# Performance work log

Measured on AMD Instinct MI355X. Metric: run time of the kernel, lower is better.

Reference implementation:

```python
import jax, jax.numpy as jnp
import numpy as np

N_EMBD = 1024
N_HEAD = 16
HEAD_DIM = N_EMBD // N_HEAD


def setup_inputs() -> dict:
    key = jax.random.key(0)
    k1, k2, k3, k4, k5 = jax.random.split(key, 5)
    x = jax.random.normal(k1, (4, 2048, N_EMBD), dtype=jnp.float32)
    s = 1.0 / np.sqrt(N_EMBD)
    W_attn = jax.random.normal(k2, (N_EMBD, 3 * N_EMBD), dtype=jnp.float32) * s
    b_attn = jnp.zeros((3 * N_EMBD,), dtype=jnp.float32)
    W_proj = jax.random.normal(k3, (N_EMBD, N_EMBD), dtype=jnp.float32) * s
    b_proj = jnp.zeros((N_EMBD,), dtype=jnp.float32)
    return {"x": x, "W_attn": W_attn, "b_attn": b_attn, "W_proj": W_proj, "b_proj": b_proj}


def _attention(x, W_attn, b_attn, W_proj, b_proj):
    B, T, C = x.shape
    qkv = jnp.einsum("btc,cd->btd", x, W_attn) + b_attn  # [B,T,3C]
    q, k, v = jnp.split(qkv, 3, axis=-1)
    # [B,T,C] -> [B,H,T,D]
    def heads(t):
        return t.reshape(B, T, N_HEAD, HEAD_DIM).transpose(0, 2, 1, 3)
    q, k, v = heads(q), heads(k), heads(v)
    scale = 1.0 / np.sqrt(HEAD_DIM)
    scores = jnp.einsum("bhqd,bhkd->bhqk", q, k) * scale  # [B,H,T,T]
    causal = jnp.tril(jnp.ones((T, T), dtype=bool))
    scores = jnp.where(causal, scores, jnp.finfo(scores.dtype).min)
    attn = jax.nn.softmax(scores, axis=-1)
    y = jnp.einsum("bhqk,bhkd->bhqd", attn, v)  # [B,H,T,D]
    y = y.transpose(0, 2, 1, 3).reshape(B, T, C)
    return jnp.einsum("btc,cd->btd", y, W_proj) + b_proj


def reference(x, W_attn, b_attn, W_proj, b_proj):
    return _attention(x, W_attn, b_attn, W_proj, b_proj)
```

## Files before the change

kernel.cpp:

```cpp
#include <hip/hip_runtime.h>
#include <hip/hip_bf16.h>

#define BB 4
#define TT 2048
#define CC 1024
#define HH 16
#define DD 64
#define BT (BB*TT)
#define C3 (3*CC)
#define LDST 72
#define QSCALE 0.18033688011112042f

typedef __attribute__((ext_vector_type(8))) short short8;
typedef __attribute__((ext_vector_type(4))) float f32x4;

__device__ __forceinline__ short f2bs(float f) {
  __hip_bfloat16 h = __float2bfloat16(f);
  return *reinterpret_cast<short*>(&h);
}

__device__ __forceinline__ void gl_lds16(const short* g, short* l) {
  __builtin_amdgcn_global_load_lds(
      (const __attribute__((address_space(1))) void*)(g),
      (__attribute__((address_space(3))) void*)(l), 16, 0, 0);
}

__global__ __launch_bounds__(256)
void prep(const float* __restrict__ Wa, short* __restrict__ Wat,
          const float* __restrict__ Wp, short* __restrict__ Wpt,
          const float* __restrict__ x, short* __restrict__ Xb)
{
  __shared__ float Lt[64][65];
  const int bx = blockIdx.x;
  if (bx >= 64) {
    size_t chunk = (size_t)(bx - 64) * 16 + blockIdx.y;
    size_t i = (chunk * 256 + threadIdx.x) * 8;
    float4 a = *reinterpret_cast<const float4*>(x + i);
    float4 b = *reinterpret_cast<const float4*>(x + i + 4);
    short8 o;
    o[0] = f2bs(a.x); o[1] = f2bs(a.y); o[2] = f2bs(a.z); o[3] = f2bs(a.w);
    o[4] = f2bs(b.x); o[5] = f2bs(b.y); o[6] = f2bs(b.z); o[7] = f2bs(b.w);
    *reinterpret_cast<short8*>(Xb + i) = o;
    return;
  }
  const bool isA = (bx < 48);
  const float* in  = isA ? Wa  : Wp;
  short*       out = isA ? Wat : Wpt;
  const int N  = isA ? C3 : CC;
  const int n0 = (isA ? bx : bx - 48) * 64;
  const int k0 = blockIdx.y * 64;
  const int cx = threadIdx.x & 15, rr = threadIdx.x >> 4;
#pragma unroll
  for (int p = 0; p < 4; ++p) {
    int kr = p * 16 + rr;
    float4 u = *reinterpret_cast<const float4*>(in + (size_t)(k0 + kr) * N + n0 + cx * 4);
    Lt[kr][cx * 4 + 0] = u.x;
    Lt[kr][cx * 4 + 1] = u.y;
    Lt[kr][cx * 4 + 2] = u.z;
    Lt[kr][cx * 4 + 3] = u.w;
  }
  __syncthreads();
#pragma unroll
  for (int p = 0; p < 4; ++p) {
    int nr = p * 16 + rr;
    short4 o;
    o.x = f2bs(Lt[cx * 4 + 0][nr]);
    o.y = f2bs(Lt[cx * 4 + 1][nr]);
    o.z = f2bs(Lt[cx * 4 + 2][nr]);
    o.w = f2bs(Lt[cx * 4 + 3][nr]);
    *reinterpret_cast<short4*>(out + (size_t)(n0 + nr) * CC + k0 + cx * 4) = o;
  }
}

template<bool QKV, int NBF>
__global__ __launch_bounds__(512, 2)
void gemm256(const short* __restrict__ A, const short* __restrict__ Bt,
             const float* __restrict__ bias,
             short* __restrict__ qb, short* __restrict__ kb, short* __restrict__ vb,
             float* __restrict__ out)
{
  constexpr int BQ   = NBF * 64 * 32;
  constexpr int BOFF = 32768;
  __shared__ __align__(16) short SMEM[BOFF + 4 * BQ];

  const int t = threadIdx.x;
  const int lane = t & 63;
  const int l16 = lane & 15, quad = lane >> 4;
  const int w = t >> 6;
  const int wr = w >> 2, wc = w & 3;

  const int per   = gridDim.x >> 3;
  const int chunk = (blockIdx.x & 7) * per + (blockIdx.x >> 3);
  const int NBC   = QKV ? 12 : (CC / (NBF * 64));
  const int brow  = chunk / NBC, bcol = chunk % NBC;
  const int row0  = brow * 256;
  const int col0  = bcol * (NBF * 64);

  auto stageQA = [&](int bufS, int kcS, int tileS) __attribute__((always_inline)) {
#pragma unroll
    for (int l = 0; l < 2; ++l) {
      int gq = l * 512 + t;
      int rq = gq >> 2;
      int g  = (gq & 3) ^ ((rq >> 1) & 3);
      gl_lds16(A + (size_t)(row0 + rq) * CC + tileS * 64 + kcS * 32 + g * 8,
               &SMEM[bufS * 16384 + kcS * 8192 + gq * 8]);
    }
  };
  auto stageQB = [&](int bufS, int kcS, int tileS) __attribute__((always_inline)) {
#pragma unroll
    for (int l = 0; l < NBF / 2; ++l) {
      int gq = l * 512 + t;
      int rq = gq >> 2;
      int g  = (gq & 3) ^ ((rq >> 1) & 3);
      gl_lds16(Bt + (size_t)(col0 + rq) * CC + tileS * 64 + kcS * 32 + g * 8,
               &SMEM[BOFF + bufS * 2 * BQ + kcS * BQ + gq * 8]);
    }
  };

  f32x4 acc[8][NBF];
#pragma unroll
  for (int i = 0; i < 8; ++i)
#pragma unroll
    for (int j = 0; j < NBF; ++j) acc[i][j] = (f32x4){0.f, 0.f, 0.f, 0.f};

  auto kTile = [&](int u, int cb, int tm) __attribute__((always_inline)) {
    const short* Ac = &SMEM[cb * 16384];
    const short* Bc = &SMEM[BOFF + cb * 2 * BQ];
    short8 bf[NBF];
#pragma unroll
    for (int ph = 0; ph < 4; ++ph) {
      const int kc = ph >> 1, q = ph & 1;
      if (q == 0) {
#pragma unroll
        for (int j = 0; j < NBF; ++j) {
          int rb = wc * (NBF * 16) + j * 16 + l16;
          bf[j] = *reinterpret_cast<const short8*>(
              &Bc[kc * BQ + rb * 32 + (((quad ^ (rb >> 1)) & 3) << 3)]);
        }
      }
      short8 af[4];
#pragma unroll
      for (int iq = 0; iq < 4; ++iq) {
        int ra = wr * 128 + (q * 4 + iq) * 16 + l16;
        af[iq] = *reinterpret_cast<const short8*>(
            &Ac[kc * 8192 + ra * 32 + (((quad ^ (ra >> 1)) & 3) << 3)]);
      }

      if      (ph == 0) { if (tm < 2) stageQA(cb ^ 1, 1, u + 1); }
      else if (ph == 1) { if (tm < 2) stageQB(cb ^ 1, 1, u + 1); }
      else if (ph == 2) { if (tm < 1) stageQA(cb,     0, u + 2); }
      else              { if (tm < 1) stageQB(cb,     0, u + 2); }

      __builtin_amdgcn_s_barrier();
      asm volatile("s_waitcnt lgkmcnt(0)" ::: "memory");
      __builtin_amdgcn_sched_barrier(0);

      __builtin_amdgcn_s_setprio(1);
#pragma unroll
      for (int iq = 0; iq < 4; ++iq)
#pragma unroll
        for (int j = 0; j < NBF; ++j)
          acc[q * 4 + iq][j] =
              __builtin_amdgcn_mfma_f32_16x16x32_bf16(af[iq], bf[j], acc[q * 4 + iq][j], 0, 0, 0);
      __builtin_amdgcn_s_setprio(0);

      if (ph == 1) {
        if (tm == 2) { asm volatile("s_waitcnt vmcnt(0)" ::: "memory"); }
        else if (NBF == 4) { asm volatile("s_waitcnt vmcnt(8)" ::: "memory"); }
        else               { asm volatile("s_waitcnt vmcnt(6)" ::: "memory"); }
      } else if (ph == 3) {
        if (tm == 0) {
          if (NBF == 4) { asm volatile("s_waitcnt vmcnt(8)" ::: "memory"); }
          else          { asm volatile("s_waitcnt vmcnt(6)" ::: "memory"); }
        } else if (tm == 1) {
          if (NBF == 4) { asm volatile("s_waitcnt vmcnt(4)" ::: "memory"); }
          else          { asm volatile("s_waitcnt vmcnt(3)" ::: "memory"); }
        }
      }
      __builtin_amdgcn_s_barrier();
    }
  };

  stageQA(0, 0, 0);  stageQB(0, 0, 0);
  stageQA(0, 1, 0);  stageQB(0, 1, 0);
  stageQA(1, 0, 1);  stageQB(1, 0, 1);
  if (NBF == 4) { asm volatile("s_waitcnt vmcnt(8)" ::: "memory"); }
  else          { asm volatile("s_waitcnt vmcnt(6)" ::: "memory"); }
  __builtin_amdgcn_s_barrier();

  for (int u = 0; u < 14; u += 2) {
    kTile(u,     0, 0);
    kTile(u + 1, 1, 0);
  }
  kTile(14, 0, 1);
  kTile(15, 1, 2);

  if constexpr (QKV) {
    const int sel = col0 >> 10;
#pragma unroll
    for (int hp = 0; hp < 2; ++hp) {
      __syncthreads();
      if (wr == hp) {
#pragma unroll
        for (int j = 0; j < 4; ++j) {
          const int colL = wc * 64 + j * 16 + l16;
          const float bv = bias[col0 + colL];
#pragma unroll
          for (int i = 0; i < 8; ++i)
#pragma unroll
            for (int r = 0; r < 4; ++r) {
              const int rl = i * 16 + quad * 4 + r;
              float val = acc[i][j][r] + bv;
              if (sel == 0) val *= QSCALE;
              short vs = f2bs(val);
              if (sel == 2) {
                int tpl = (rl & ~63) | ((rl & 15) << 2) | ((rl >> 4) & 3);
                SMEM[colL * 136 + tpl] = vs;
              } else {
                SMEM[rl * 264 + colL] = vs;
              }
            }
        }
      }
      __syncthreads();
      const int Rbase = row0 + hp * 128;
      const int bi = Rbase >> 11;
      if (sel == 0) {
#pragma unroll
        for (int rep = 0; rep < 8; ++rep) {
          int slot = rep * 512 + t;
          int rl = slot >> 5, ch = slot & 31;
          short8 vv = *reinterpret_cast<const short8*>(&SMEM[rl * 264 + ch * 8]);
          int tt  = (Rbase & 2047) + rl;
          int cin = (col0 + ch * 8) & 1023;
          int hh = cin >> 6, dd = cin & 63;
          *reinterpret_cast<short8*>(
              &qb[(((size_t)(bi * HH + hh)) * TT + tt) * DD + dd]) = vv;
        }
      } else if (sel == 1) {
#pragma unroll
        for (int rep = 0; rep < 8; ++rep) {
          int slot = rep * 512 + t;
          int rl = slot >> 5, ch = slot & 31;
          short8 vv = *reinterpret_cast<const short8*>(&SMEM[rl * 264 + ch * 8]);
          int tt  = (Rbase & 2047) + rl;
          int cin = (col0 + ch * 8) & 1023;
          int hh = cin >> 6;
          int rt = tt & 63;
          int cs = ((cin >> 3) & 7) ^ ((rt >> 1) & 7);
          size_t tile = (size_t)(bi * HH + hh) * 32 + (tt >> 6);
          *reinterpret_cast<short8*>(&kb[tile * 4096 + rt * 64 + cs * 8]) = vv;
        }
      } else {
#pragma unroll
        for (int rep = 0; rep < 8; ++rep) {
          int slot = rep * 512 + t;
          int dcol = slot >> 4, ch = slot & 15;
          short8 vv = *reinterpret_cast<const short8*>(&SMEM[dcol * 136 + ch * 8]);
          int cin = (col0 + dcol) & 1023;
          int hh = cin >> 6, dd = cin & 63;
          int ktv = ((Rbase & 2047) >> 6) + (ch >> 3);
          int cs  = (ch & 7) ^ ((dd >> 1) & 7);
          *reinterpret_cast<short8*>(
              &vb[((size_t)(bi * HH + hh) * 32 + ktv) * 4096 + dd * 64 + cs * 8]) = vv;
        }
      }
    }
  } else {
#pragma unroll
    for (int j = 0; j < NBF; ++j) {
      int col = col0 + wc * (NBF * 16) + j * 16 + l16;
      float bv = bias[col];
#pragma unroll
      for (int i = 0; i < 8; ++i)
#pragma unroll
        for (int r = 0; r < 4; ++r) {
          int row = row0 + wr * 128 + i * 16 + quad * 4 + r;
          out[(size_t)row * CC + col] = acc[i][j][r] + bv;
        }
    }
  }
}

__global__ __launch_bounds__(256, 4)
void attn_mfma(const short* __restrict__ Qb, const short* __restrict__ Kb,
               const short* __restrict__ Vb, short* __restrict__ Y)
{
  __shared__ __align__(16) short Kd[2][4096];
  __shared__ __align__(16) short Vt[4096];
  __shared__ __align__(16) short Pw[4 * 16 * LDST];

  const int t    = threadIdx.x;
  const int w    = t >> 6;
  const int lane = t & 63;
  const int l16  = lane & 15;
  const int quad = lane >> 4;

  const int linear = blockIdx.x + 16 * (blockIdx.y + 16 * blockIdx.z);
  const int nb  = (linear & 7) * 128 + (linear >> 3);
  const int qt0 = nb & 15;
  const int h   = (nb >> 4) & 15;
  const int bi  = nb >> 8;
  const size_t head = (size_t)(bi * HH + h) * TT * DD;

  short* myP = &Pw[w * 16 * LDST];

  auto stageK = [&](int kt, int p) __attribute__((always_inline)) {
    const short* src = Kb + head + (size_t)kt * 4096;
    gl_lds16(src + t * 8,        &Kd[p][t * 8]);
    gl_lds16(src + 2048 + t * 8, &Kd[p][2048 + t * 8]);
  };
  auto stageV = [&](int kt) __attribute__((always_inline)) {
    const short* src = Vb + head + (size_t)kt * 4096;
    gl_lds16(src + t * 8,        &Vt[t * 8]);
    gl_lds16(src + 2048 + t * 8, &Vt[2048 + t * 8]);
  };

  const int qts[2] = { qt0, 31 - qt0 };

#pragma unroll
  for (int half = 0; half < 2; ++half) {
    const int qt = qts[half];
    const int q0 = qt * 64;

    short8 qf[2];
#pragma unroll
    for (int kc = 0; kc < 2; ++kc)
      qf[kc] = *reinterpret_cast<const short8*>(
          &Qb[head + (size_t)(q0 + w * 16 + l16) * DD + kc * 32 + quad * 8]);

    f32x4 O[4];
#pragma unroll
    for (int dt = 0; dt < 4; ++dt) O[dt] = (f32x4){0.f, 0.f, 0.f, 0.f};
    float lsum[4] = {};

    stageK(0, 0);
    stageV(0);
    if (qt >= 1) {
      stageK(1, 1);
      asm volatile("s_waitcnt vmcnt(4)" ::: "memory");
    } else {
      asm volatile("s_waitcnt vmcnt(2)" ::: "memory");
    }
    __builtin_amdgcn_s_barrier();

    for (int kt = 0; kt <= qt; ++kt) {
      const int p  = kt & 1;
      const int k0 = kt * 64;

      short8 kf[4][2];
#pragma unroll
      for (int nt = 0; nt < 4; ++nt)
#pragma unroll
        for (int kc = 0; kc < 2; ++kc) {
          int r = nt * 16 + l16;
          int c = kc * 4 + quad;
          kf[nt][kc] = *reinterpret_cast<const short8*>(
              &Kd[p][r * 64 + ((c ^ ((r >> 1) & 7)) << 3)]);
        }

      f32x4 s[4];
#pragma unroll
      for (int nt = 0; nt < 4; ++nt) s[nt] = (f32x4){0.f, 0.f, 0.f, 0.f};
      __builtin_amdgcn_s_setprio(1);
#pragma unroll
      for (int nt = 0; nt < 4; ++nt)
#pragma unroll
        for (int kc = 0; kc < 2; ++kc)
          s[nt] = __builtin_amdgcn_mfma_f32_16x16x32_bf16(qf[kc], kf[nt][kc], s[nt], 0, 0, 0);
      __builtin_amdgcn_s_setprio(0);

      const int rowg_base = q0 + w * 16 + quad * 4;
#pragma unroll
      for (int r = 0; r < 4; ++r) {
        const int rowg = rowg_base + r;
        short pk[4];
#pragma unroll
        for (int nt = 0; nt < 4; ++nt) {
          float e = (k0 + nt * 16 + l16 <= rowg) ? __builtin_amdgcn_exp2f(s[nt][r]) : 0.f;
          lsum[r] += e;
          pk[nt] = f2bs(e);
        }
        short4 p4; p4.x = pk[0]; p4.y = pk[1]; p4.z = pk[2]; p4.w = pk[3];
        *reinterpret_cast<short4*>(&myP[(quad * 4 + r) * LDST + (l16 << 2)]) = p4;
      }

      asm volatile("s_waitcnt vmcnt(0)" ::: "memory");
      __builtin_amdgcn_s_barrier();

      if (kt + 2 <= qt) stageK(kt + 2, p);

      __builtin_amdgcn_s_setprio(1);
#pragma unroll
      for (int cc = 0; cc < 2; ++cc) {
        short8 pf = *reinterpret_cast<const short8*>(
            &myP[l16 * LDST + cc * 32 + quad * 8]);
#pragma unroll
        for (int dt = 0; dt < 4; ++dt) {
          int r = dt * 16 + l16;
          int c = cc * 4 + quad;
          short8 vf = *reinterpret_cast<const short8*>(
              &Vt[r * 64 + ((c ^ ((r >> 1) & 7)) << 3)]);
          O[dt] = __builtin_amdgcn_mfma_f32_16x16x32_bf16(pf, vf, O[dt], 0, 0, 0);
        }
      }
      __builtin_amdgcn_s_setprio(0);

      __builtin_amdgcn_s_barrier();
      if (kt + 1 <= qt) stageV(kt + 1);
    }

    float linv[4];
#pragma unroll
    for (int r = 0; r < 4; ++r) {
      float s = lsum[r];
      s += __shfl_xor(s, 1);
      s += __shfl_xor(s, 2);
      s += __shfl_xor(s, 4);
      s += __shfl_xor(s, 8);
      linv[r] = 1.f / s;
    }
#pragma unroll
    for (int dt = 0; dt < 4; ++dt)
#pragma unroll
      for (int r = 0; r < 4; ++r) {
        int tg = q0 + w * 16 + quad * 4 + r;
        Y[((size_t)bi * TT + tg) * CC + h * DD + dt * 16 + l16] =
            f2bs(O[dt][r] * linv[r]);
      }
  }
}

extern "C" void kernel_launch(void* const* d_in, const int* in_sizes, int n_in,
                              void* d_out, int out_size, void* d_ws, size_t ws_size,
                              hipStream_t stream) {
  const float* x  = (const float*)d_in[0];
  const float* Wa = (const float*)d_in[1];
  const float* ba = (const float*)d_in[2];
  const float* Wp = (const float*)d_in[3];
  const float* bp = (const float*)d_in[4];
  float* out = (float*)d_out;

  const size_t NELT = (size_t)BB * HH * TT * DD;
  short* qb  = (short*)d_ws;
  short* kb  = qb + NELT;
  short* vb  = kb + NELT;
  short* Xb  = vb + NELT;
  short* Wat = Xb  + (size_t)BT * CC;
  short* Wpt = Wat + (size_t)CC * C3;
  short* Yb  = Wpt + (size_t)CC * CC;

  prep<<<dim3(64 + 256, 16), 256, 0, stream>>>(Wa, Wat, Wp, Wpt, x, Xb);

  gemm256<true, 4> <<<dim3((C3 / 256) * (BT / 256)), 512, 0, stream>>>(Xb, Wat, ba, qb, kb, vb, nullptr);
  attn_mfma        <<<dim3(16, HH, BB),              256, 0, stream>>>(qb, kb, vb, Yb);
  gemm256<false, 2><<<dim3((CC / 128) * (BT / 256)), 512, 0, stream>>>(Yb, Wpt, bp, nullptr, nullptr, nullptr, out);
}
```

Baseline: 250.9 us.

## Enlarge attention query tile to 128 rows per block to reuse K/V tiles

```diff
diff --git a/kernel.cpp b/kernel.cpp
--- a/kernel.cpp
+++ b/kernel.cpp
@@ -282,13 +282,13 @@
   }
 }
 
-__global__ __launch_bounds__(256, 4)
+__global__ __launch_bounds__(256, 2)
 void attn_mfma(const short* __restrict__ Qb, const short* __restrict__ Kb,
                const short* __restrict__ Vb, short* __restrict__ Y)
 {
   __shared__ __align__(16) short Kd[2][4096];
   __shared__ __align__(16) short Vt[4096];
-  __shared__ __align__(16) short Pw[4 * 16 * LDST];
+  __shared__ __align__(16) short Pw[4 * 32 * LDST];
 
   const int t    = threadIdx.x;
   const int w    = t >> 6;
@@ -296,14 +296,14 @@
   const int l16  = lane & 15;
   const int quad = lane >> 4;
 
-  const int linear = blockIdx.x + 16 * (blockIdx.y + 16 * blockIdx.z);
-  const int nb  = (linear & 7) * 128 + (linear >> 3);
-  const int qt0 = nb & 15;
-  const int h   = (nb >> 4) & 15;
-  const int bi  = nb >> 8;
+  const int linear = blockIdx.x + 8 * (blockIdx.y + 16 * blockIdx.z);
+  const int nb  = (linear & 7) * 64 + (linear >> 3);
+  const int qb0 = nb & 7;
+  const int h   = (nb >> 3) & 15;
+  const int bi  = nb >> 7;
   const size_t head = (size_t)(bi * HH + h) * TT * DD;
 
-  short* myP = &Pw[w * 16 * LDST];
+  short* myP = &Pw[w * 32 * LDST];
 
   auto stageK = [&](int kt, int p) __attribute__((always_inline)) {
     const short* src = Kb + head + (size_t)kt * 4096;
@@ -316,35 +316,36 @@
     gl_lds16(src + 2048 + t * 8, &Vt[2048 + t * 8]);
   };
 
-  const int qts[2] = { qt0, 31 - qt0 };
+  const int qbs[2] = { qb0, 15 - qb0 };
 
 #pragma unroll
   for (int half = 0; half < 2; ++half) {
-    const int qt = qts[half];
-    const int q0 = qt * 64;
-
-    short8 qf[2];
-#pragma unroll
-    for (int kc = 0; kc < 2; ++kc)
-      qf[kc] = *reinterpret_cast<const short8*>(
-          &Qb[head + (size_t)(q0 + w * 16 + l16) * DD + kc * 32 + quad * 8]);
-
-    f32x4 O[4];
-#pragma unroll
-    for (int dt = 0; dt < 4; ++dt) O[dt] = (f32x4){0.f, 0.f, 0.f, 0.f};
-    float lsum[4] = {};
+    const int qb  = qbs[half];
+    const int q0  = qb * 128;
+    const int nkt = 2 * qb + 2;
+
+    short8 qf[2][2];
+#pragma unroll
+    for (int i = 0; i < 2; ++i)
+#pragma unroll
+      for (int kc = 0; kc < 2; ++kc)
+        qf[i][kc] = *reinterpret_cast<const short8*>(
+            &Qb[head + (size_t)(q0 + w * 32 + i * 16 + l16) * DD + kc * 32 + quad * 8]);
+
+    f32x4 O[2][4];
+#pragma unroll
+    for (int i = 0; i < 2; ++i)
+#pragma unroll
+      for (int dt = 0; dt < 4; ++dt) O[i][dt] = (f32x4){0.f, 0.f, 0.f, 0.f};
+    float lsum[2][4] = {};
 
     stageK(0, 0);
     stageV(0);
-    if (qt >= 1) {
-      stageK(1, 1);
-      asm volatile("s_waitcnt vmcnt(4)" ::: "memory");
-    } else {
-      asm volatile("s_waitcnt vmcnt(2)" ::: "memory");
-    }
+    stageK(1, 1);
+    asm volatile("s_waitcnt vmcnt(4)" ::: "memory");
     __builtin_amdgcn_s_barrier();
 
-    for (int kt = 0; kt <= qt; ++kt) {
+    for (int kt = 0; kt < nkt; ++kt) {
       const int p  = kt & 1;
       const int k0 = kt * 64;
 
@@ -359,75 +360,91 @@
               &Kd[p][r * 64 + ((c ^ ((r >> 1) & 7)) << 3)]);
         }
 
-      f32x4 s[4];
-#pragma unroll
-      for (int nt = 0; nt < 4; ++nt) s[nt] = (f32x4){0.f, 0.f, 0.f, 0.f};
+      f32x4 s[2][4];
+#pragma unroll
+      for (int i = 0; i < 2; ++i)
+#pragma unroll
+        for (int nt = 0; nt < 4; ++nt) s[i][nt] = (f32x4){0.f, 0.f, 0.f, 0.f};
       __builtin_amdgcn_s_setprio(1);
 #pragma unroll
-      for (int nt = 0; nt < 4; ++nt)
-#pragma unroll
-        for (int kc = 0; kc < 2; ++kc)
-          s[nt] = __builtin_amdgcn_mfma_f32_16x16x32_bf16(qf[kc], kf[nt][kc], s[nt], 0, 0, 0);
+      for (int i = 0; i < 2; ++i)
+#pragma unroll
+        for (int nt = 0; nt < 4; ++nt)
+#pragma unroll
+          for (int kc = 0; kc < 2; ++kc)
+            s[i][nt] = __builtin_amdgcn_mfma_f32_16x16x32_bf16(qf[i][kc], kf[nt][kc], s[i][nt], 0, 0, 0);
       __builtin_amdgcn_s_setprio(0);
 
-      const int rowg_base = q0 + w * 16 + quad * 4;
-#pragma unroll
-      for (int r = 0; r < 4; ++r) {
-        const int rowg = rowg_base + r;
-        short pk[4];
-#pragma unroll
-        for (int nt = 0; nt < 4; ++nt) {
-          float e = (k0 + nt * 16 + l16 <= rowg) ? __builtin_amdgcn_exp2f(s[nt][r]) : 0.f;
-          lsum[r] += e;
-          pk[nt] = f2bs(e);
-        }
-        short4 p4; p4.x = pk[0]; p4.y = pk[1]; p4.z = pk[2]; p4.w = pk[3];
-        *reinterpret_cast<short4*>(&myP[(quad * 4 + r) * LDST + (l16 << 2)]) = p4;
+#pragma unroll
+      for (int i = 0; i < 2; ++i) {
+        const int rowg_base = q0 + w * 32 + i * 16 + quad * 4;
+#pragma unroll
+        for (int r = 0; r < 4; ++r) {
+          const int rowg = rowg_base + r;
+          short pk[4];
+#pragma unroll
+          for (int nt = 0; nt < 4; ++nt) {
+            float e = (k0 + nt * 16 + l16 <= rowg) ? __builtin_amdgcn_exp2f(s[i][nt][r]) : 0.f;
+            lsum[i][r] += e;
+            pk[nt] = f2bs(e);
+          }
+          short4 p4; p4.x = pk[0]; p4.y = pk[1]; p4.z = pk[2]; p4.w = pk[3];
+          *reinterpret_cast<short4*>(&myP[(i * 16 + quad * 4 + r) * LDST + (l16 << 2)]) = p4;
+        }
       }
 
       asm volatile("s_waitcnt vmcnt(0)" ::: "memory");
       __builtin_amdgcn_s_barrier();
 
-      if (kt + 2 <= qt) stageK(kt + 2, p);
+      if (kt + 2 < nkt) stageK(kt + 2, p);
 
       __builtin_amdgcn_s_setprio(1);
 #pragma unroll
       for (int cc = 0; cc < 2; ++cc) {
-        short8 pf = *reinterpret_cast<const short8*>(
-            &myP[l16 * LDST + cc * 32 + quad * 8]);
+        short8 pf[2];
+#pragma unroll
+        for (int i = 0; i < 2; ++i)
+          pf[i] = *reinterpret_cast<const short8*>(
+              &myP[(i * 16 + l16) * LDST + cc * 32 + quad * 8]);
 #pragma unroll
         for (int dt = 0; dt < 4; ++dt) {
           int r = dt * 16 + l16;
           int c = cc * 4 + quad;
           short8 vf = *reinterpret_cast<const short8*>(
               &Vt[r * 64 + ((c ^ ((r >> 1) & 7)) << 3)]);
-          O[dt] = __builtin_amdgcn_mfma_f32_16x16x32_bf16(pf, vf, O[dt], 0, 0, 0);
+#pragma unroll
+          for (int i = 0; i < 2; ++i)
+            O[i][dt] = __builtin_amdgcn_mfma_f32_16x16x32_bf16(pf[i], vf, O[i][dt], 0, 0, 0);
         }
       }
       __builtin_amdgcn_s_setprio(0);
 
       __builtin_amdgcn_s_barrier();
-      if (kt + 1 <= qt) stageV(kt + 1);
-    }
-
-    float linv[4];
-#pragma unroll
-    for (int r = 0; r < 4; ++r) {
-      float s = lsum[r];
-      s += __shfl_xor(s, 1);
-      s += __shfl_xor(s, 2);
-      s += __shfl_xor(s, 4);
-      s += __shfl_xor(s, 8);
-      linv[r] = 1.f / s;
-    }
-#pragma unroll
-    for (int dt = 0; dt < 4; ++dt)
+      if (kt + 1 < nkt) stageV(kt + 1);
+    }
+
+    float linv[2][4];
+#pragma unroll
+    for (int i = 0; i < 2; ++i)
 #pragma unroll
       for (int r = 0; r < 4; ++r) {
-        int tg = q0 + w * 16 + quad * 4 + r;
-        Y[((size_t)bi * TT + tg) * CC + h * DD + dt * 16 + l16] =
-            f2bs(O[dt][r] * linv[r]);
-      }
+        float s = lsum[i][r];
+        s += __shfl_xor(s, 1);
+        s += __shfl_xor(s, 2);
+        s += __shfl_xor(s, 4);
+        s += __shfl_xor(s, 8);
+        linv[i][r] = 1.f / s;
+      }
+#pragma unroll
+    for (int i = 0; i < 2; ++i)
+#pragma unroll
+      for (int dt = 0; dt < 4; ++dt)
+#pragma unroll
+        for (int r = 0; r < 4; ++r) {
+          int tg = q0 + w * 32 + i * 16 + quad * 4 + r;
+          Y[((size_t)bi * TT + tg) * CC + h * DD + dt * 16 + l16] =
+              f2bs(O[i][dt][r] * linv[i][r]);
+        }
   }
 }
 
@@ -453,6 +470,6 @@
   prep<<<dim3(64 + 256, 16), 256, 0, stream>>>(Wa, Wat, Wp, Wpt, x, Xb);
 
   gemm256<true, 4> <<<dim3((C3 / 256) * (BT / 256)), 512, 0, stream>>>(Xb, Wat, ba, qb, kb, vb, nullptr);
-  attn_mfma        <<<dim3(16, HH, BB),              256, 0, stream>>>(qb, kb, vb, Yb);
+  attn_mfma        <<<dim3(8, HH, BB),               256, 0, stream>>>(qb, kb, vb, Yb);
   gemm256<false, 2><<<dim3((CC / 128) * (BT / 256)), 512, 0, stream>>>(Yb, Wpt, bp, nullptr, nullptr, nullptr, out);
 }
```

After: 254.2 us. About the same (+1.3%).
